# Kernel optimization log

Measured on AMD Instinct MI355X. Metric: run time of the kernel, lower is better.

## Reference

```python
import jax, jax.numpy as jnp
import numpy as np

B, R, U, D = 16, 2048, 2048, 1024
EPS_ATT = 1e-8
EPS_LN = 1e-6


def setup_inputs() -> dict:
    key = jax.random.key(0)
    ks = jax.random.split(key, 6)
    s = 1.0 / np.sqrt(D)
    return {
        "Q": jax.random.normal(ks[0], (B, R, D), dtype=jnp.float32),
        "K": jax.random.normal(ks[1], (B, U, D), dtype=jnp.float32),
        "V": jax.random.normal(ks[2], (B, U, D), dtype=jnp.float32),
        "W1": jax.random.normal(ks[3], (D, D), dtype=jnp.float32) * s,
        "b1": jnp.zeros((D,), dtype=jnp.float32),
        "W2": jax.random.normal(ks[4], (D, D), dtype=jnp.float32) * s,
        "b2": jnp.zeros((D,), dtype=jnp.float32),
        "gamma": jnp.ones((D,), dtype=jnp.float32),
        "beta": jnp.zeros((D,), dtype=jnp.float32),
    }


def reference(Q, K, V, W1, b1, W2, b2, gamma, beta):
    d_model = Q.shape[-1]
    # Faithful to source: sqrt(d_model + epsilon)
    scale = jnp.sqrt(jnp.asarray(d_model, jnp.float32) + EPS_ATT)
    scores = jnp.einsum('brd,bud->bru', Q, K) / scale  # [B,R,U]
    att = jax.nn.softmax(scores, axis=-1)
    V_att = jnp.einsum('bru,bud->brd', att, V)  # [B,R,D]

    def layer_norm(x):
        mu = jnp.mean(x, axis=-1, keepdims=True)
        var = jnp.mean(jnp.square(x - mu), axis=-1, keepdims=True)
        return gamma * (x - mu) / jnp.sqrt(var + EPS_LN) + beta

    X = layer_norm(Q + V_att)
    ffn = jnp.maximum(X @ W1 + b1, 0.0) @ W2 + b2
    return layer_norm(ffn + X)
```

## Files before the change

### kernel.cpp

```cpp
#include <hip/hip_runtime.h>
#include <math.h>
#include <stdint.h>

#define BATCH 16
#define RDIM 2048
#define UDIM 2048
#define DDIM 1024

typedef __attribute__((ext_vector_type(8))) short short8;
typedef __attribute__((ext_vector_type(4))) float f32x4;
typedef __attribute__((ext_vector_type(8))) unsigned short ushort8;
typedef __attribute__((ext_vector_type(4))) unsigned short ushort4v;
typedef __attribute__((ext_vector_type(4))) float float4v;

__device__ __forceinline__ float bf2f(unsigned short u) {
  unsigned int x = ((unsigned int)u) << 16;
  return __builtin_bit_cast(float, x);
}
__device__ __forceinline__ unsigned short f2bf(float f) {
  unsigned int x = __builtin_bit_cast(unsigned int, f);
  unsigned int r = (x + 0x7fffu + ((x >> 16) & 1u)) >> 16;
  return (unsigned short)r;
}

__device__ __forceinline__ void gload_lds16(const void* g, void* l) {
  __builtin_amdgcn_global_load_lds(
      (const __attribute__((address_space(1))) void*)(uintptr_t)g,
      (__attribute__((address_space(3))) void*)(uint32_t)(uintptr_t)l,
      16, 0, 0);
}

#define FENCE() __builtin_amdgcn_sched_barrier(0)
#define BAR() __builtin_amdgcn_s_barrier()
#define LGKM0() asm volatile("s_waitcnt lgkmcnt(0)" ::: "memory")
#define LGKM4() asm volatile("s_waitcnt lgkmcnt(4)" ::: "memory")
#define LGKM8() asm volatile("s_waitcnt lgkmcnt(8)" ::: "memory")
#define VMCNT0() asm volatile("s_waitcnt vmcnt(0)" ::: "memory")


__global__ __launch_bounds__(256) void k_conv_bf16(const float* __restrict__ in,
                                                   unsigned short* __restrict__ out,
                                                   float scale) {
  const long i = ((long)blockIdx.x * 256 + threadIdx.x) * 8;
  float4v a = *(const float4v*)(in + i);
  float4v b = *(const float4v*)(in + i + 4);
  ushort8 o;
#pragma unroll
  for (int j = 0; j < 4; ++j) o[j] = f2bf(a[j] * scale);
#pragma unroll
  for (int j = 0; j < 4; ++j) o[4 + j] = f2bf(b[j] * scale);
  *(ushort8*)(out + i) = o;
}

__global__ void k_transpose_bf16(const float* __restrict__ in,
                                 unsigned short* __restrict__ out,
                                 int rows, int cols, long sIn, long sOut) {
  __shared__ unsigned short tile[64][65];
  const long bz = blockIdx.z;
  in += bz * sIn;
  out += bz * sOut;
  const int r0 = blockIdx.x * 64;
  const int c0 = blockIdx.y * 64;
  const int tx = threadIdx.x;
  const int ty = threadIdx.y;
#pragma unroll
  for (int i = 0; i < 16; ++i) {
    const int r = ty + i * 4;
    tile[r][tx] = f2bf(in[(long)(r0 + r) * cols + c0 + tx]);
  }
  __syncthreads();
#pragma unroll
  for (int i = 0; i < 16; ++i) {
    const int r = ty + i * 4;
    out[(long)(c0 + r) * rows + r0 + tx] = tile[tx][r];
  }
}


template <int EPI>
__global__ __launch_bounds__(512, 2) void gemm_bt(
    const unsigned short* __restrict__ A, const unsigned short* __restrict__ B,
    void* __restrict__ Cout, int N, int K, long sA, long sB, long sC,
    const float* __restrict__ bias, const unsigned short* __restrict__ res) {
  __shared__ __align__(128) unsigned short lds[2][2][2][256 * 32];

  int lin = blockIdx.x + gridDim.x * (blockIdx.y + gridDim.y * blockIdx.z);
  lin = (lin & 7) * ((gridDim.x * gridDim.y * gridDim.z) >> 3) + (lin >> 3);
  const int by = lin % gridDim.y;
  int rest = lin / gridDim.y;
  const int bx = rest % gridDim.x;
  const int bz = rest / gridDim.x;

  const unsigned short* Ab = A + (long)bz * sA;
  const unsigned short* Bb = B + (long)bz * sB;

  const int tid = threadIdx.x;
  const int w = tid >> 6;
  const int lane = tid & 63;
  const int wm = w >> 2;
  const int wn = w & 3;
  const long rowBase = (long)bx * 256;
  const long colBase = (long)by * 256;

  const int stRow = w * 16 + (lane >> 2);
  const int stKc = ((lane & 3) ^ ((lane >> 3) & 3)) << 3;
  const unsigned short* gA = Ab + (rowBase + stRow) * (long)K + stKc;
  const unsigned short* gB = Bb + (colBase + stRow) * (long)K + stKc;
  const long qStep = (long)128 * K;
  char* ldsB = (char*)&lds[0][0][0][0];
  const int dOff = w * 1024;

  auto STAGE = [&](int buf, int op, int ks, int kadd) {
    const unsigned short* g = (op == 0 ? gA : gB) + kadd;
    char* d = ldsB + ((buf * 4 + op * 2 + ks) << 14) + dOff;
    gload_lds16(g, d);
    gload_lds16(g + qStep, d + 8192);
  };

  const int laneM = lane & 15;
  const int laneQ = lane >> 4;
  const int swz = (laneQ ^ ((laneM >> 1) & 3)) << 4;
  const int rdA = (wm * 128 + laneM) * 64 + swz;
  const int rdB = (wn * 64 + laneM) * 64 + swz;

  f32x4 acc[8][4] = {};
  const int NT = K >> 6;
  const int NTm1 = NT - 1;

  STAGE(0, 0, 0, 0);
  STAGE(0, 0, 1, 32);
  STAGE(0, 1, 0, 0);
  STAGE(0, 1, 1, 32);
  VMCNT0();
  BAR();
  FENCE();

  for (int t = 0; t < NT; ++t) {
    const int cur = t & 1;
    const int nxt = cur ^ 1;
    const int sA0 = (cur * 4 + 0) << 14;
    const int sA1 = (cur * 4 + 1) << 14;
    const int sB0 = (cur * 4 + 2) << 14;
    const int sB1 = (cur * 4 + 3) << 14;
    const int tn = (t + 1 <= NTm1 ? t + 1 : NTm1);
    const int ka = tn * 64;

    short8 a0[4], a1[4], a2[4], a3[4], b0[4], b1[4];

#pragma unroll
    for (int m = 0; m < 4; ++m)
      a0[m] = *(const short8*)(ldsB + sA0 + rdA + m * 1024);
#pragma unroll
    for (int n = 0; n < 4; ++n)
      b0[n] = *(const short8*)(ldsB + sB0 + rdB + n * 1024);
    FENCE();
#pragma unroll
    for (int m = 0; m < 4; ++m)
      a1[m] = *(const short8*)(ldsB + sA0 + rdA + (4 + m) * 1024);
    STAGE(nxt, 0, 0, ka);
    STAGE(nxt, 0, 1, ka + 32);
    LGKM4();
    FENCE();
    __builtin_amdgcn_s_setprio(1);
#pragma unroll
    for (int m = 0; m < 4; ++m)
#pragma unroll
      for (int n = 0; n < 4; ++n)
        acc[m][n] = __builtin_amdgcn_mfma_f32_16x16x32_bf16(a0[m], b0[n],
                                                            acc[m][n], 0, 0, 0);
    __builtin_amdgcn_s_setprio(0);

#pragma unroll
    for (int m = 0; m < 4; ++m)
      a2[m] = *(const short8*)(ldsB + sA1 + rdA + m * 1024);
#pragma unroll
    for (int n = 0; n < 4; ++n)
      b1[n] = *(const short8*)(ldsB + sB1 + rdB + n * 1024);
    STAGE(nxt, 1, 0, ka);
    STAGE(nxt, 1, 1, ka + 32);
    LGKM8();
    FENCE();
    __builtin_amdgcn_s_setprio(1);
#pragma unroll
    for (int m = 0; m < 4; ++m)
#pragma unroll
      for (int n = 0; n < 4; ++n)
        acc[4 + m][n] = __builtin_amdgcn_mfma_f32_16x16x32_bf16(a1[m], b0[n],
                                                                acc[4 + m][n], 0, 0, 0);
    __builtin_amdgcn_s_setprio(0);

#pragma unroll
    for (int m = 0; m < 4; ++m)
      a3[m] = *(const short8*)(ldsB + sA1 + rdA + (4 + m) * 1024);
    LGKM4();
    FENCE();
    __builtin_amdgcn_s_setprio(1);
#pragma unroll
    for (int m = 0; m < 4; ++m)
#pragma unroll
      for (int n = 0; n < 4; ++n)
        acc[m][n] = __builtin_amdgcn_mfma_f32_16x16x32_bf16(a2[m], b1[n],
                                                            acc[m][n], 0, 0, 0);
    __builtin_amdgcn_s_setprio(0);

    LGKM0();
    FENCE();
    __builtin_amdgcn_s_setprio(1);
#pragma unroll
    for (int m = 0; m < 4; ++m)
#pragma unroll
      for (int n = 0; n < 4; ++n)
        acc[4 + m][n] = __builtin_amdgcn_mfma_f32_16x16x32_bf16(a3[m], b1[n],
                                                                acc[4 + m][n], 0, 0, 0);
    __builtin_amdgcn_s_setprio(0);
    FENCE();
    VMCNT0();
    BAR();
    FENCE();
  }

  const long r0 = rowBase + wm * 128;
  const long c0 = colBase + wn * 64;
  const int cr = (lane >> 4) << 2;
  const int cc = lane & 15;

  if constexpr (EPI == 0) {
    unsigned short* C = (unsigned short*)Cout + (long)bz * sC;
#pragma unroll
    for (int i = 0; i < 8; ++i)
#pragma unroll
      for (int j = 0; j < 4; ++j)
#pragma unroll
        for (int jj = 0; jj < 4; ++jj)
          C[(r0 + i * 16 + cr + jj) * N + (c0 + j * 16 + cc)] = f2bf(acc[i][j][jj]);
  } else if constexpr (EPI == 1) {
    unsigned short* C = (unsigned short*)Cout;
#pragma unroll
    for (int i = 0; i < 8; ++i)
#pragma unroll
      for (int j = 0; j < 4; ++j)
#pragma unroll
        for (int jj = 0; jj < 4; ++jj) {
          const long col = c0 + j * 16 + cc;
          float v = acc[i][j][jj] + bias[col];
          v = fmaxf(v, 0.f);
          C[(r0 + i * 16 + cr + jj) * N + col] = f2bf(v);
        }
  } else {
    float* C = (float*)Cout;
#pragma unroll
    for (int i = 0; i < 8; ++i)
#pragma unroll
      for (int j = 0; j < 4; ++j)
#pragma unroll
        for (int jj = 0; jj < 4; ++jj) {
          const long row = r0 + i * 16 + cr + jj;
          const long col = c0 + j * 16 + cc;
          C[row * N + col] = acc[i][j][jj] + bias[col] + bf2f(res[row * N + col]);
        }
  }
}


__global__ __launch_bounds__(256) void k_softmax(unsigned short* __restrict__ S) {
  __shared__ float red[8];
  const long base = (long)blockIdx.x * UDIM;
  const int t = threadIdx.x;
  ushort8 raw = *(const ushort8*)(S + base + t * 8);
  float v[8];
  float mx = -3.0e38f;
#pragma unroll
  for (int j = 0; j < 8; ++j) {
    v[j] = bf2f(raw[j]);
    mx = fmaxf(mx, v[j]);
  }
#pragma unroll
  for (int m = 32; m >= 1; m >>= 1) mx = fmaxf(mx, __shfl_xor(mx, m));
  const int wv = t >> 6;
  if ((t & 63) == 0) red[wv] = mx;
  __syncthreads();
  mx = fmaxf(fmaxf(red[0], red[1]), fmaxf(red[2], red[3]));
  float s = 0.f;
#pragma unroll
  for (int j = 0; j < 8; ++j) {
    v[j] = __expf(v[j] - mx);
    s += v[j];
  }
#pragma unroll
  for (int m = 32; m >= 1; m >>= 1) s += __shfl_xor(s, m);
  if ((t & 63) == 0) red[4 + wv] = s;
  __syncthreads();
  s = red[4] + red[5] + red[6] + red[7];
  const float rs = 1.f / s;
  ushort8 o;
#pragma unroll
  for (int j = 0; j < 8; ++j) o[j] = f2bf(v[j] * rs);
  *(ushort8*)(S + base + t * 8) = o;
}


__global__ __launch_bounds__(256) void k_addln_bf16(
    const float* __restrict__ Q, const unsigned short* __restrict__ Va,
    unsigned short* __restrict__ X, const float* __restrict__ gamma,
    const float* __restrict__ beta) {
  __shared__ float red[8];
  const long base = (long)blockIdx.x * DDIM;
  const int t = threadIdx.x;
  float4v q = *(const float4v*)(Q + base + t * 4);
  ushort4v a = *(const ushort4v*)(Va + base + t * 4);
  float x[4];
  float s = 0.f, ss = 0.f;
#pragma unroll
  for (int j = 0; j < 4; ++j) {
    x[j] = q[j] + bf2f(a[j]);
    s += x[j];
    ss += x[j] * x[j];
  }
#pragma unroll
  for (int m = 32; m >= 1; m >>= 1) {
    s += __shfl_xor(s, m);
    ss += __shfl_xor(ss, m);
  }
  const int wv = t >> 6;
  if ((t & 63) == 0) {
    red[wv] = s;
    red[4 + wv] = ss;
  }
  __syncthreads();
  s = red[0] + red[1] + red[2] + red[3];
  ss = red[4] + red[5] + red[6] + red[7];
  const float mu = s * (1.f / DDIM);
  const float var = ss * (1.f / DDIM) - mu * mu;
  const float rstd = rsqrtf(var + 1e-6f);
  ushort4v o;
#pragma unroll
  for (int j = 0; j < 4; ++j) {
    const int c = t * 4 + j;
    o[j] = f2bf(gamma[c] * ((x[j] - mu) * rstd) + beta[c]);
  }
  *(ushort4v*)(X + base + t * 4) = o;
}


__global__ __launch_bounds__(256) void k_ln_inplace(float* __restrict__ Y,
                                                    const float* __restrict__ gamma,
                                                    const float* __restrict__ beta) {
  __shared__ float red[8];
  const long base = (long)blockIdx.x * DDIM;
  const int t = threadIdx.x;
  float4v y = *(const float4v*)(Y + base + t * 4);
  float s = 0.f, ss = 0.f;
#pragma unroll
  for (int j = 0; j < 4; ++j) {
    s += y[j];
    ss += y[j] * y[j];
  }
#pragma unroll
  for (int m = 32; m >= 1; m >>= 1) {
    s += __shfl_xor(s, m);
    ss += __shfl_xor(ss, m);
  }
  const int wv = t >> 6;
  if ((t & 63) == 0) {
    red[wv] = s;
    red[4 + wv] = ss;
  }
  __syncthreads();
  s = red[0] + red[1] + red[2] + red[3];
  ss = red[4] + red[5] + red[6] + red[7];
  const float mu = s * (1.f / DDIM);
  const float var = ss * (1.f / DDIM) - mu * mu;
  const float rstd = rsqrtf(var + 1e-6f);
  float4v o;
#pragma unroll
  for (int j = 0; j < 4; ++j) {
    const int c = t * 4 + j;
    o[j] = gamma[c] * ((y[j] - mu) * rstd) + beta[c];
  }
  *(float4v*)(Y + base + t * 4) = o;
}


extern "C" void kernel_launch(void* const* d_in, const int* in_sizes, int n_in,
                              void* d_out, int out_size, void* d_ws, size_t ws_size,
                              hipStream_t stream) {
  const float* Q = (const float*)d_in[0];
  const float* Kin = (const float*)d_in[1];
  const float* V = (const float*)d_in[2];
  const float* W1 = (const float*)d_in[3];
  const float* b1 = (const float*)d_in[4];
  const float* W2 = (const float*)d_in[5];
  const float* b2 = (const float*)d_in[6];
  const float* gamma = (const float*)d_in[7];
  const float* beta = (const float*)d_in[8];
  float* out = (float*)d_out;

  const long nQ = (long)BATCH * RDIM * DDIM;
  const long nK = (long)BATCH * UDIM * DDIM;
  const long nS = (long)BATCH * RDIM * UDIM;

  char* w = (char*)d_ws;
  unsigned short* Qb = (unsigned short*)w;  w += nQ * 2;
  unsigned short* Kb = (unsigned short*)w;  w += nK * 2;
  unsigned short* Vt = (unsigned short*)w;  w += nK * 2;
  unsigned short* S  = (unsigned short*)w;  w += nS * 2;
  unsigned short* X  = (unsigned short*)w;  w += nQ * 2;
  unsigned short* W1t = (unsigned short*)w; w += (long)DDIM * DDIM * 2;
  unsigned short* W2t = (unsigned short*)w; w += (long)DDIM * DDIM * 2;
  unsigned short* Va = Qb;
  unsigned short* H  = S;

  const float scale = 1.0f / sqrtf(1024.0f + 1e-8f);

  k_conv_bf16<<<nQ / 2048, 256, 0, stream>>>(Q, Qb, scale);
  k_conv_bf16<<<nK / 2048, 256, 0, stream>>>(Kin, Kb, 1.0f);
  k_transpose_bf16<<<dim3(UDIM / 64, DDIM / 64, BATCH), dim3(64, 4), 0, stream>>>(
      V, Vt, UDIM, DDIM, (long)UDIM * DDIM, (long)UDIM * DDIM);
  k_transpose_bf16<<<dim3(DDIM / 64, DDIM / 64, 1), dim3(64, 4), 0, stream>>>(
      W1, W1t, DDIM, DDIM, 0, 0);
  k_transpose_bf16<<<dim3(DDIM / 64, DDIM / 64, 1), dim3(64, 4), 0, stream>>>(
      W2, W2t, DDIM, DDIM, 0, 0);

  gemm_bt<0><<<dim3(RDIM / 256, UDIM / 256, BATCH), 512, 0, stream>>>(
      Qb, Kb, S, UDIM, DDIM, (long)RDIM * DDIM, (long)UDIM * DDIM, (long)RDIM * UDIM,
      nullptr, nullptr);
  k_softmax<<<BATCH * RDIM, 256, 0, stream>>>(S);
  gemm_bt<0><<<dim3(RDIM / 256, DDIM / 256, BATCH), 512, 0, stream>>>(
      S, Vt, Va, DDIM, UDIM, (long)RDIM * UDIM, (long)DDIM * UDIM, (long)RDIM * DDIM,
      nullptr, nullptr);
  k_addln_bf16<<<BATCH * RDIM, 256, 0, stream>>>(Q, Va, X, gamma, beta);
  gemm_bt<1><<<dim3(BATCH * RDIM / 256, DDIM / 256, 1), 512, 0, stream>>>(
      X, W1t, H, DDIM, DDIM, 0, 0, 0, b1, nullptr);
  gemm_bt<2><<<dim3(BATCH * RDIM / 256, DDIM / 256, 1), 512, 0, stream>>>(
      H, W2t, out, DDIM, DDIM, 0, 0, 0, b2, X);
  k_ln_inplace<<<BATCH * RDIM, 256, 0, stream>>>(out, gamma, beta);
}
```

Before: 665.6 us.

## Shrink GEMM tiles to 128x128 with 4 waves and 32x32x16 MFMA

The bf16 GEMM kernel moves from 256x256 tiles with 8 waves issuing 16x16x32 MFMAs to 128x128 tiles with 4 waves issuing 32x32x16 MFMAs, each wave computing a 64x64 sub-tile. LDS staging, swizzled read offsets, the prefetch schedule and the epilogue index mapping are rewritten to match the new fragment layout. The goal is to cut LDS read traffic per MFMA flop and to use smaller blocks for better occupancy. In exchange, the smaller tiles double global reads per output, and the pipeline now waits on both k-halves before computing.

```diff
diff --git a/kernel.cpp b/kernel.cpp
--- a/kernel.cpp
+++ b/kernel.cpp
@@ -8,7 +8,7 @@
 #define DDIM 1024
 
 typedef __attribute__((ext_vector_type(8))) short short8;
-typedef __attribute__((ext_vector_type(4))) float f32x4;
+typedef __attribute__((ext_vector_type(16))) float f32x16;
 typedef __attribute__((ext_vector_type(8))) unsigned short ushort8;
 typedef __attribute__((ext_vector_type(4))) unsigned short ushort4v;
 typedef __attribute__((ext_vector_type(4))) float float4v;
@@ -33,7 +33,6 @@
 #define FENCE() __builtin_amdgcn_sched_barrier(0)
 #define BAR() __builtin_amdgcn_s_barrier()
 #define LGKM0() asm volatile("s_waitcnt lgkmcnt(0)" ::: "memory")
-#define LGKM4() asm volatile("s_waitcnt lgkmcnt(4)" ::: "memory")
 #define LGKM8() asm volatile("s_waitcnt lgkmcnt(8)" ::: "memory")
 #define VMCNT0() asm volatile("s_waitcnt vmcnt(0)" ::: "memory")
 
@@ -78,11 +77,11 @@
 
 
 template <int EPI>
-__global__ __launch_bounds__(512, 2) void gemm_bt(
+__global__ __launch_bounds__(256, 2) void gemm_bt(
     const unsigned short* __restrict__ A, const unsigned short* __restrict__ B,
     void* __restrict__ Cout, int N, int K, long sA, long sB, long sC,
     const float* __restrict__ bias, const unsigned short* __restrict__ res) {
-  __shared__ __align__(128) unsigned short lds[2][2][2][256 * 32];
+  __shared__ __align__(128) unsigned short lds[2][2][2][128 * 32];
 
   int lin = blockIdx.x + gridDim.x * (blockIdx.y + gridDim.y * blockIdx.z);
   lin = (lin & 7) * ((gridDim.x * gridDim.y * gridDim.z) >> 3) + (lin >> 3);
@@ -97,33 +96,35 @@
   const int tid = threadIdx.x;
   const int w = tid >> 6;
   const int lane = tid & 63;
-  const int wm = w >> 2;
-  const int wn = w & 3;
-  const long rowBase = (long)bx * 256;
-  const long colBase = (long)by * 256;
+  const int wm = w >> 1;
+  const int wn = w & 1;
+  const long rowBase = (long)bx * 128;
+  const long colBase = (long)by * 128;
 
   const int stRow = w * 16 + (lane >> 2);
   const int stKc = ((lane & 3) ^ ((lane >> 3) & 3)) << 3;
   const unsigned short* gA = Ab + (rowBase + stRow) * (long)K + stKc;
   const unsigned short* gB = Bb + (colBase + stRow) * (long)K + stKc;
-  const long qStep = (long)128 * K;
+  const long qStep = (long)64 * K;
   char* ldsB = (char*)&lds[0][0][0][0];
   const int dOff = w * 1024;
 
   auto STAGE = [&](int buf, int op, int ks, int kadd) {
     const unsigned short* g = (op == 0 ? gA : gB) + kadd;
-    char* d = ldsB + ((buf * 4 + op * 2 + ks) << 14) + dOff;
+    char* d = ldsB + ((buf * 4 + op * 2 + ks) << 13) + dOff;
     gload_lds16(g, d);
-    gload_lds16(g + qStep, d + 8192);
+    gload_lds16(g + qStep, d + 4096);
   };
 
-  const int laneM = lane & 15;
-  const int laneQ = lane >> 4;
-  const int swz = (laneQ ^ ((laneM >> 1) & 3)) << 4;
-  const int rdA = (wm * 128 + laneM) * 64 + swz;
-  const int rdB = (wn * 64 + laneM) * 64 + swz;
-
-  f32x4 acc[8][4] = {};
+  const int r = lane & 31;
+  const int h = lane >> 5;
+  const int rsw = (r >> 1) & 3;
+  const int co0 = ((h ^ rsw) << 4);
+  const int co1 = (((2 | h) ^ rsw) << 4);
+  const int rdA = (wm * 64 + r) * 64;
+  const int rdB = (wn * 64 + r) * 64;
+
+  f32x16 acc[2][2] = {};
   const int NT = K >> 6;
   const int NTm1 = NT - 1;
 
@@ -138,80 +139,63 @@
   for (int t = 0; t < NT; ++t) {
     const int cur = t & 1;
     const int nxt = cur ^ 1;
-    const int sA0 = (cur * 4 + 0) << 14;
-    const int sA1 = (cur * 4 + 1) << 14;
-    const int sB0 = (cur * 4 + 2) << 14;
-    const int sB1 = (cur * 4 + 3) << 14;
+    const int sA0 = (cur * 4 + 0) << 13;
+    const int sA1 = (cur * 4 + 1) << 13;
+    const int sB0 = (cur * 4 + 2) << 13;
+    const int sB1 = (cur * 4 + 3) << 13;
     const int tn = (t + 1 <= NTm1 ? t + 1 : NTm1);
     const int ka = tn * 64;
 
-    short8 a0[4], a1[4], a2[4], a3[4], b0[4], b1[4];
-
-#pragma unroll
-    for (int m = 0; m < 4; ++m)
-      a0[m] = *(const short8*)(ldsB + sA0 + rdA + m * 1024);
-#pragma unroll
-    for (int n = 0; n < 4; ++n)
-      b0[n] = *(const short8*)(ldsB + sB0 + rdB + n * 1024);
+    short8 a0[2][2], b0[2][2], a1[2][2], b1[2][2];
+
+#pragma unroll
+    for (int m = 0; m < 2; ++m) {
+      a0[m][0] = *(const short8*)(ldsB + sA0 + rdA + m * 2048 + co0);
+      a0[m][1] = *(const short8*)(ldsB + sA0 + rdA + m * 2048 + co1);
+    }
+#pragma unroll
+    for (int n = 0; n < 2; ++n) {
+      b0[n][0] = *(const short8*)(ldsB + sB0 + rdB + n * 2048 + co0);
+      b0[n][1] = *(const short8*)(ldsB + sB0 + rdB + n * 2048 + co1);
+    }
     FENCE();
 #pragma unroll
-    for (int m = 0; m < 4; ++m)
-      a1[m] = *(const short8*)(ldsB + sA0 + rdA + (4 + m) * 1024);
+    for (int m = 0; m < 2; ++m) {
+      a1[m][0] = *(const short8*)(ldsB + sA1 + rdA + m * 2048 + co0);
+      a1[m][1] = *(const short8*)(ldsB + sA1 + rdA + m * 2048 + co1);
+    }
+#pragma unroll
+    for (int n = 0; n < 2; ++n) {
+      b1[n][0] = *(const short8*)(ldsB + sB1 + rdB + n * 2048 + co0);
+      b1[n][1] = *(const short8*)(ldsB + sB1 + rdB + n * 2048 + co1);
+    }
     STAGE(nxt, 0, 0, ka);
     STAGE(nxt, 0, 1, ka + 32);
-    LGKM4();
-    FENCE();
-    __builtin_amdgcn_s_setprio(1);
-#pragma unroll
-    for (int m = 0; m < 4; ++m)
-#pragma unroll
-      for (int n = 0; n < 4; ++n)
-        acc[m][n] = __builtin_amdgcn_mfma_f32_16x16x32_bf16(a0[m], b0[n],
-                                                            acc[m][n], 0, 0, 0);
-    __builtin_amdgcn_s_setprio(0);
-
-#pragma unroll
-    for (int m = 0; m < 4; ++m)
-      a2[m] = *(const short8*)(ldsB + sA1 + rdA + m * 1024);
-#pragma unroll
-    for (int n = 0; n < 4; ++n)
-      b1[n] = *(const short8*)(ldsB + sB1 + rdB + n * 1024);
-    STAGE(nxt, 1, 0, ka);
-    STAGE(nxt, 1, 1, ka + 32);
     LGKM8();
     FENCE();
     __builtin_amdgcn_s_setprio(1);
 #pragma unroll
-    for (int m = 0; m < 4; ++m)
-#pragma unroll
-      for (int n = 0; n < 4; ++n)
-        acc[4 + m][n] = __builtin_amdgcn_mfma_f32_16x16x32_bf16(a1[m], b0[n],
-                                                                acc[4 + m][n], 0, 0, 0);
+    for (int ks = 0; ks < 2; ++ks)
+#pragma unroll
+      for (int m = 0; m < 2; ++m)
+#pragma unroll
+        for (int n = 0; n < 2; ++n)
+          acc[m][n] = __builtin_amdgcn_mfma_f32_32x32x16_bf16(
+              a0[m][ks], b0[n][ks], acc[m][n], 0, 0, 0);
     __builtin_amdgcn_s_setprio(0);
-
-#pragma unroll
-    for (int m = 0; m < 4; ++m)
-      a3[m] = *(const short8*)(ldsB + sA1 + rdA + (4 + m) * 1024);
-    LGKM4();
-    FENCE();
-    __builtin_amdgcn_s_setprio(1);
-#pragma unroll
-    for (int m = 0; m < 4; ++m)
-#pragma unroll
-      for (int n = 0; n < 4; ++n)
-        acc[m][n] = __builtin_amdgcn_mfma_f32_16x16x32_bf16(a2[m], b1[n],
-                                                            acc[m][n], 0, 0, 0);
-    __builtin_amdgcn_s_setprio(0);
-
+    STAGE(nxt, 1, 0, ka);
+    STAGE(nxt, 1, 1, ka + 32);
     LGKM0();
     FENCE();
     __builtin_amdgcn_s_setprio(1);
 #pragma unroll
-    for (int m = 0; m < 4; ++m)
-#pragma unroll
-      for (int n = 0; n < 4; ++n)
-        acc[4 + m][n] = __builtin_amdgcn_mfma_f32_16x16x32_bf16(a3[m], b1[n],
-                                                                acc[4 + m][n], 0, 0, 0);
+    for (int ks = 0; ks < 2; ++ks)
+#pragma unroll
+      for (int m = 0; m < 2; ++m)
+#pragma unroll
+        for (int n = 0; n < 2; ++n)
+          acc[m][n] = __builtin_amdgcn_mfma_f32_32x32x16_bf16(
+              a1[m][ks], b1[n][ks], acc[m][n], 0, 0, 0);
     __builtin_amdgcn_s_setprio(0);
     FENCE();
     VMCNT0();
@@ -219,44 +203,46 @@
     FENCE();
   }
 
-  const long r0 = rowBase + wm * 128;
+  const long r0 = rowBase + wm * 64;
   const long c0 = colBase + wn * 64;
-  const int cr = (lane >> 4) << 2;
-  const int cc = lane & 15;
 
   if constexpr (EPI == 0) {
     unsigned short* C = (unsigned short*)Cout + (long)bz * sC;
 #pragma unroll
-    for (int i = 0; i < 8; ++i)
-#pragma unroll
-      for (int j = 0; j < 4; ++j)
-#pragma unroll
-        for (int jj = 0; jj < 4; ++jj)
-          C[(r0 + i * 16 + cr + jj) * N + (c0 + j * 16 + cc)] = f2bf(acc[i][j][jj]);
+    for (int m = 0; m < 2; ++m)
+#pragma unroll
+      for (int n = 0; n < 2; ++n)
+#pragma unroll
+        for (int j = 0; j < 16; ++j) {
+          const long row = r0 + m * 32 + (j & 3) + 8 * (j >> 2) + 4 * h;
+          const long col = c0 + n * 32 + r;
+          C[row * N + col] = f2bf(acc[m][n][j]);
+        }
   } else if constexpr (EPI == 1) {
     unsigned short* C = (unsigned short*)Cout;
 #pragma unroll
-    for (int i = 0; i < 8; ++i)
-#pragma unroll
-      for (int j = 0; j < 4; ++j)
-#pragma unroll
-        for (int jj = 0; jj < 4; ++jj) {
-          const long col = c0 + j * 16 + cc;
-          float v = acc[i][j][jj] + bias[col];
+    for (int m = 0; m < 2; ++m)
+#pragma unroll
+      for (int n = 0; n < 2; ++n)
+#pragma unroll
+        for (int j = 0; j < 16; ++j) {
+          const long row = r0 + m * 32 + (j & 3) + 8 * (j >> 2) + 4 * h;
+          const long col = c0 + n * 32 + r;
+          float v = acc[m][n][j] + bias[col];
           v = fmaxf(v, 0.f);
-          C[(r0 + i * 16 + cr + jj) * N + col] = f2bf(v);
+          C[row * N + col] = f2bf(v);
         }
   } else {
     float* C = (float*)Cout;
 #pragma unroll
-    for (int i = 0; i < 8; ++i)
-#pragma unroll
-      for (int j = 0; j < 4; ++j)
-#pragma unroll
-        for (int jj = 0; jj < 4; ++jj) {
-          const long row = r0 + i * 16 + cr + jj;
-          const long col = c0 + j * 16 + cc;
-          C[row * N + col] = acc[i][j][jj] + bias[col] + bf2f(res[row * N + col]);
+    for (int m = 0; m < 2; ++m)
+#pragma unroll
+      for (int n = 0; n < 2; ++n)
+#pragma unroll
+        for (int j = 0; j < 16; ++j) {
+          const long row = r0 + m * 32 + (j & 3) + 8 * (j >> 2) + 4 * h;
+          const long col = c0 + n * 32 + r;
+          C[row * N + col] = acc[m][n][j] + bias[col] + bf2f(res[row * N + col]);
         }
   }
 }
@@ -421,17 +407,17 @@
   k_transpose_bf16<<<dim3(DDIM / 64, DDIM / 64, 1), dim3(64, 4), 0, stream>>>(
       W2, W2t, DDIM, DDIM, 0, 0);
 
-  gemm_bt<0><<<dim3(RDIM / 256, UDIM / 256, BATCH), 512, 0, stream>>>(
+  gemm_bt<0><<<dim3(RDIM / 128, UDIM / 128, BATCH), 256, 0, stream>>>(
       Qb, Kb, S, UDIM, DDIM, (long)RDIM * DDIM, (long)UDIM * DDIM, (long)RDIM * UDIM,
       nullptr, nullptr);
   k_softmax<<<BATCH * RDIM, 256, 0, stream>>>(S);
-  gemm_bt<0><<<dim3(RDIM / 256, DDIM / 256, BATCH), 512, 0, stream>>>(
+  gemm_bt<0><<<dim3(RDIM / 128, DDIM / 128, BATCH), 256, 0, stream>>>(
       S, Vt, Va, DDIM, UDIM, (long)RDIM * UDIM, (long)DDIM * UDIM, (long)RDIM * DDIM,
       nullptr, nullptr);
   k_addln_bf16<<<BATCH * RDIM, 256, 0, stream>>>(Q, Va, X, gamma, beta);
-  gemm_bt<1><<<dim3(BATCH * RDIM / 256, DDIM / 256, 1), 512, 0, stream>>>(
+  gemm_bt<1><<<dim3(BATCH * RDIM / 128, DDIM / 128, 1), 256, 0, stream>>>(
       X, W1t, H, DDIM, DDIM, 0, 0, 0, b1, nullptr);
-  gemm_bt<2><<<dim3(BATCH * RDIM / 256, DDIM / 256, 1), 512, 0, stream>>>(
+  gemm_bt<2><<<dim3(BATCH * RDIM / 128, DDIM / 128, 1), 256, 0, stream>>>(
       H, W2t, out, DDIM, DDIM, 0, 0, 0, b2, X);
   k_ln_inplace<<<BATCH * RDIM, 256, 0, stream>>>(out, gamma, beta);
 }
```

Result: slower. 799.7 us (+20.1%).

## Use 4-wave GEMM blocks with 128x128 per-wave tiles and simpler pipeline

Applied to the files above, without the earlier changes.

Reworks the bf16 GEMM kernel from 8 waves (2x4, 128x64 per wave) to 4 waves (2x2, 128x128 per wave) for the same 256x256 block tile. Each wave now issues twice as many global-to-LDS loads and keeps an 8x8 accumulator array, which raises register reuse per LDS fragment. The four-phase interleaved LDS read/MFMA schedule becomes two phases with all fragments preloaded. This greatly increases register pressure (256 accumulator VGPRs plus 32 fragment registers) and cuts waves per CU, risking spills or less latency hiding.

```diff
diff --git a/kernel.cpp b/kernel.cpp
--- a/kernel.cpp
+++ b/kernel.cpp
@@ -33,8 +33,7 @@
 #define FENCE() __builtin_amdgcn_sched_barrier(0)
 #define BAR() __builtin_amdgcn_s_barrier()
 #define LGKM0() asm volatile("s_waitcnt lgkmcnt(0)" ::: "memory")
-#define LGKM4() asm volatile("s_waitcnt lgkmcnt(4)" ::: "memory")
-#define LGKM8() asm volatile("s_waitcnt lgkmcnt(8)" ::: "memory")
+#define LGKM15() asm volatile("s_waitcnt lgkmcnt(15)" ::: "memory")
 #define VMCNT0() asm volatile("s_waitcnt vmcnt(0)" ::: "memory")
 
 
@@ -78,7 +77,7 @@
 
 
 template <int EPI>
-__global__ __launch_bounds__(512, 2) void gemm_bt(
+__global__ __launch_bounds__(256, 1) void gemm_bt(
     const unsigned short* __restrict__ A, const unsigned short* __restrict__ B,
     void* __restrict__ Cout, int N, int K, long sA, long sB, long sC,
     const float* __restrict__ bias, const unsigned short* __restrict__ res) {
@@ -97,8 +96,8 @@
   const int tid = threadIdx.x;
   const int w = tid >> 6;
   const int lane = tid & 63;
-  const int wm = w >> 2;
-  const int wn = w & 3;
+  const int wm = w >> 1;
+  const int wn = w & 1;
   const long rowBase = (long)bx * 256;
   const long colBase = (long)by * 256;
 
@@ -106,7 +105,7 @@
   const int stKc = ((lane & 3) ^ ((lane >> 3) & 3)) << 3;
   const unsigned short* gA = Ab + (rowBase + stRow) * (long)K + stKc;
   const unsigned short* gB = Bb + (colBase + stRow) * (long)K + stKc;
-  const long qStep = (long)128 * K;
+  const long qStep = (long)64 * K;
   char* ldsB = (char*)&lds[0][0][0][0];
   const int dOff = w * 1024;
 
@@ -114,16 +113,18 @@
     const unsigned short* g = (op == 0 ? gA : gB) + kadd;
     char* d = ldsB + ((buf * 4 + op * 2 + ks) << 14) + dOff;
     gload_lds16(g, d);
-    gload_lds16(g + qStep, d + 8192);
+    gload_lds16(g + qStep, d + 4096);
+    gload_lds16(g + 2 * qStep, d + 8192);
+    gload_lds16(g + 3 * qStep, d + 12288);
   };
 
   const int laneM = lane & 15;
   const int laneQ = lane >> 4;
   const int swz = (laneQ ^ ((laneM >> 1) & 3)) << 4;
   const int rdA = (wm * 128 + laneM) * 64 + swz;
-  const int rdB = (wn * 64 + laneM) * 64 + swz;
-
-  f32x4 acc[8][4] = {};
+  const int rdB = (wn * 128 + laneM) * 64 + swz;
+
+  f32x4 acc[8][8] = {};
   const int NT = K >> 6;
   const int NTm1 = NT - 1;
 
@@ -145,73 +146,44 @@
     const int tn = (t + 1 <= NTm1 ? t + 1 : NTm1);
     const int ka = tn * 64;
 
-    short8 a0[4], a1[4], a2[4], a3[4], b0[4], b1[4];
-
-#pragma unroll
-    for (int m = 0; m < 4; ++m)
+    short8 a0[8], b0[8], a1[8], b1[8];
+
+#pragma unroll
+    for (int m = 0; m < 8; ++m)
       a0[m] = *(const short8*)(ldsB + sA0 + rdA + m * 1024);
 #pragma unroll
-    for (int n = 0; n < 4; ++n)
+    for (int n = 0; n < 8; ++n)
       b0[n] = *(const short8*)(ldsB + sB0 + rdB + n * 1024);
     FENCE();
 #pragma unroll
-    for (int m = 0; m < 4; ++m)
-      a1[m] = *(const short8*)(ldsB + sA0 + rdA + (4 + m) * 1024);
+    for (int m = 0; m < 8; ++m)
+      a1[m] = *(const short8*)(ldsB + sA1 + rdA + m * 1024);
+#pragma unroll
+    for (int n = 0; n < 8; ++n)
+      b1[n] = *(const short8*)(ldsB + sB1 + rdB + n * 1024);
     STAGE(nxt, 0, 0, ka);
     STAGE(nxt, 0, 1, ka + 32);
-    LGKM4();
+    LGKM15();
     FENCE();
     __builtin_amdgcn_s_setprio(1);
 #pragma unroll
-    for (int m = 0; m < 4; ++m)
-#pragma unroll
-      for (int n = 0; n < 4; ++n)
+    for (int m = 0; m < 8; ++m)
+#pragma unroll
+      for (int n = 0; n < 8; ++n)
         acc[m][n] = __builtin_amdgcn_mfma_f32_16x16x32_bf16(a0[m], b0[n],
                                                             acc[m][n], 0, 0, 0);
     __builtin_amdgcn_s_setprio(0);
-
-#pragma unroll
-    for (int m = 0; m < 4; ++m)
-      a2[m] = *(const short8*)(ldsB + sA1 + rdA + m * 1024);
-#pragma unroll
-    for (int n = 0; n < 4; ++n)
-      b1[n] = *(const short8*)(ldsB + sB1 + rdB + n * 1024);
     STAGE(nxt, 1, 0, ka);
     STAGE(nxt, 1, 1, ka + 32);
-    LGKM8();
-    FENCE();
-    __builtin_amdgcn_s_setprio(1);
-#pragma unroll
-    for (int m = 0; m < 4; ++m)
-#pragma unroll
-      for (int n = 0; n < 4; ++n)
-        acc[4 + m][n] = __builtin_amdgcn_mfma_f32_16x16x32_bf16(a1[m], b0[n],
-                                                                acc[4 + m][n], 0, 0, 0);
-    __builtin_amdgcn_s_setprio(0);
-
-#pragma unroll
-    for (int m = 0; m < 4; ++m)
-      a3[m] = *(const short8*)(ldsB + sA1 + rdA + (4 + m) * 1024);
-    LGKM4();
-    FENCE();
-    __builtin_amdgcn_s_setprio(1);
-#pragma unroll
-    for (int m = 0; m < 4; ++m)
-#pragma unroll
-      for (int n = 0; n < 4; ++n)
-        acc[m][n] = __builtin_amdgcn_mfma_f32_16x16x32_bf16(a2[m], b1[n],
-                                                            acc[m][n], 0, 0, 0);
-    __builtin_amdgcn_s_setprio(0);
-
     LGKM0();
     FENCE();
     __builtin_amdgcn_s_setprio(1);
 #pragma unroll
-    for (int m = 0; m < 4; ++m)
-#pragma unroll
-      for (int n = 0; n < 4; ++n)
-        acc[4 + m][n] = __builtin_amdgcn_mfma_f32_16x16x32_bf16(a3[m], b1[n],
-                                                                acc[4 + m][n], 0, 0, 0);
+    for (int m = 0; m < 8; ++m)
+#pragma unroll
+      for (int n = 0; n < 8; ++n)
+        acc[m][n] = __builtin_amdgcn_mfma_f32_16x16x32_bf16(a1[m], b1[n],
+                                                            acc[m][n], 0, 0, 0);
     __builtin_amdgcn_s_setprio(0);
     FENCE();
     VMCNT0();
@@ -220,7 +192,7 @@
   }
 
   const long r0 = rowBase + wm * 128;
-  const long c0 = colBase + wn * 64;
+  const long c0 = colBase + wn * 128;
   const int cr = (lane >> 4) << 2;
   const int cc = lane & 15;
 
@@ -229,7 +201,7 @@
 #pragma unroll
     for (int i = 0; i < 8; ++i)
 #pragma unroll
-      for (int j = 0; j < 4; ++j)
+      for (int j = 0; j < 8; ++j)
 #pragma unroll
         for (int jj = 0; jj < 4; ++jj)
           C[(r0 + i * 16 + cr + jj) * N + (c0 + j * 16 + cc)] = f2bf(acc[i][j][jj]);
@@ -238,7 +210,7 @@
 #pragma unroll
     for (int i = 0; i < 8; ++i)
 #pragma unroll
-      for (int j = 0; j < 4; ++j)
+      for (int j = 0; j < 8; ++j)
 #pragma unroll
         for (int jj = 0; jj < 4; ++jj) {
           const long col = c0 + j * 16 + cc;
@@ -251,7 +223,7 @@
 #pragma unroll
     for (int i = 0; i < 8; ++i)
 #pragma unroll
-      for (int j = 0; j < 4; ++j)
+      for (int j = 0; j < 8; ++j)
 #pragma unroll
         for (int jj = 0; jj < 4; ++jj) {
           const long row = r0 + i * 16 + cr + jj;
@@ -421,17 +393,17 @@
   k_transpose_bf16<<<dim3(DDIM / 64, DDIM / 64, 1), dim3(64, 4), 0, stream>>>(
       W2, W2t, DDIM, DDIM, 0, 0);
 
-  gemm_bt<0><<<dim3(RDIM / 256, UDIM / 256, BATCH), 512, 0, stream>>>(
+  gemm_bt<0><<<dim3(RDIM / 256, UDIM / 256, BATCH), 256, 0, stream>>>(
       Qb, Kb, S, UDIM, DDIM, (long)RDIM * DDIM, (long)UDIM * DDIM, (long)RDIM * UDIM,
       nullptr, nullptr);
   k_softmax<<<BATCH * RDIM, 256, 0, stream>>>(S);
-  gemm_bt<0><<<dim3(RDIM / 256, DDIM / 256, BATCH), 512, 0, stream>>>(
+  gemm_bt<0><<<dim3(RDIM / 256, DDIM / 256, BATCH), 256, 0, stream>>>(
       S, Vt, Va, DDIM, UDIM, (long)RDIM * UDIM, (long)DDIM * UDIM, (long)RDIM * DDIM,
       nullptr, nullptr);
   k_addln_bf16<<<BATCH * RDIM, 256, 0, stream>>>(Q, Va, X, gamma, beta);
-  gemm_bt<1><<<dim3(BATCH * RDIM / 256, DDIM / 256, 1), 512, 0, stream>>>(
+  gemm_bt<1><<<dim3(BATCH * RDIM / 256, DDIM / 256, 1), 256, 0, stream>>>(
       X, W1t, H, DDIM, DDIM, 0, 0, 0, b1, nullptr);
-  gemm_bt<2><<<dim3(BATCH * RDIM / 256, DDIM / 256, 1), 512, 0, stream>>>(
+  gemm_bt<2><<<dim3(BATCH * RDIM / 256, DDIM / 256, 1), 256, 0, stream>>>(
       H, W2t, out, DDIM, DDIM, 0, 0, 0, b2, X);
   k_ln_inplace<<<BATCH * RDIM, 256, 0, stream>>>(out, gamma, beta);
 }
```

Measured after the change: 776.2 us. +16.6%, slower.
